# Kernel optimization log

Measured on AMD Instinct MI355X. Metric: run time of the kernel, lower is better.

Reference implementation:

```python
import jax, jax.numpy as jnp
import numpy as np

B, N, E = 8, 2000, 32000
LAT, STY, NF = 128, 64, 10
HEADS, HID = 4, 128
OUT = 3 + NF  # 13
EPS = 1e-5
SLOPE = 0.2


def _lin(k, fi, fo):
    return jax.random.normal(k, (fi, fo), dtype=jnp.float32) / np.sqrt(fi)


def setup_inputs() -> dict:
    key = jax.random.key(0)
    ks = jax.random.split(key, 32)
    inp = {
        'z': jax.random.normal(ks[0], (B, LAT), dtype=jnp.float32),
        'template_x': jax.random.normal(ks[1], (N, NF), dtype=jnp.float32),
        'template_edge_index': jax.random.randint(ks[2], (2, E), 0, N, dtype=jnp.int32),
        # style MLP
        'mlp_w1': _lin(ks[3], LAT, 256), 'mlp_b1': jnp.zeros((256,), jnp.float32),
        'mlp_w2': _lin(ks[4], 256, 512), 'mlp_b2': jnp.zeros((512,), jnp.float32),
        'mlp_w3': _lin(ks[5], 512, STY), 'mlp_b3': jnp.zeros((STY,), jnp.float32),
        # GAT1: in = NF + STY = 74 -> heads*HID = 512, concat
        'gat1_w': _lin(ks[6], NF + STY, HEADS * HID),
        'gat1_as': jax.random.normal(ks[7], (HEADS, HID), jnp.float32) * 0.1,
        'gat1_ad': jax.random.normal(ks[8], (HEADS, HID), jnp.float32) * 0.1,
        'gat1_b': jnp.zeros((HEADS * HID,), jnp.float32),
        'ln1_g': jnp.ones((HEADS * HID,), jnp.float32), 'ln1_b': jnp.zeros((HEADS * HID,), jnp.float32),
        # GAT2: 512 -> 512, concat
        'gat2_w': _lin(ks[9], HEADS * HID, HEADS * HID),
        'gat2_as': jax.random.normal(ks[10], (HEADS, HID), jnp.float32) * 0.1,
        'gat2_ad': jax.random.normal(ks[11], (HEADS, HID), jnp.float32) * 0.1,
        'gat2_b': jnp.zeros((HEADS * HID,), jnp.float32),
        'ln2_g': jnp.ones((HEADS * HID,), jnp.float32), 'ln2_b': jnp.zeros((HEADS * HID,), jnp.float32),
        # GAT3: 512 -> 13, 1 head, no concat
        'gat3_w': _lin(ks[12], HEADS * HID, OUT),
        'gat3_as': jax.random.normal(ks[13], (1, OUT), jnp.float32) * 0.1,
        'gat3_ad': jax.random.normal(ks[14], (1, OUT), jnp.float32) * 0.1,
        'gat3_b': jnp.zeros((OUT,), jnp.float32),
    }
    return inp


def gat_conv(x, src, dst, n_nodes, W, a_src, a_dst, bias, heads, out_ch, concat):
    # x: [NT, F_in]; per-head linear transform
    h = (x @ W).reshape(-1, heads, out_ch)              # [NT, H, C]
    als = jnp.sum(h * a_src[None], axis=-1)             # [NT, H]
    ald = jnp.sum(h * a_dst[None], axis=-1)             # [NT, H]
    logits = jax.nn.leaky_relu(als[src] + ald[dst], SLOPE)   # [E, H]
    # segment softmax over destination nodes (self-loops guarantee nonempty segments)
    mx = jax.ops.segment_max(logits, dst, num_segments=n_nodes)
    alpha = jnp.exp(logits - mx[dst])
    den = jax.ops.segment_sum(alpha, dst, num_segments=n_nodes)
    alpha = alpha / den[dst]                             # [E, H]
    msgs = h[src] * alpha[:, :, None]                    # [E, H, C]
    out = jax.ops.segment_sum(msgs, dst, num_segments=n_nodes)  # [NT, H, C]
    if concat:
        return out.reshape(n_nodes, heads * out_ch) + bias
    return out.mean(axis=1) + bias


def layer_norm(x, g, b):
    mu = jnp.mean(x, axis=-1, keepdims=True)
    var = jnp.mean((x - mu) ** 2, axis=-1, keepdims=True)
    return (x - mu) * jax.lax.rsqrt(var + EPS) * g + b


def reference(z, template_x, template_edge_index,
              mlp_w1, mlp_b1, mlp_w2, mlp_b2, mlp_w3, mlp_b3,
              gat1_w, gat1_as, gat1_ad, gat1_b, ln1_g, ln1_b,
              gat2_w, gat2_as, gat2_ad, gat2_b, ln2_g, ln2_b,
              gat3_w, gat3_as, gat3_ad, gat3_b):
    bsz = z.shape[0]
    n = template_x.shape[0]
    nt = bsz * n
    # batch the template graph: replicate nodes, offset edge indices per graph
    x = jnp.tile(template_x, (bsz, 1))                                  # [NT, NF]
    off = (jnp.arange(bsz, dtype=template_edge_index.dtype) * n)
    ei = (template_edge_index[:, None, :] + off[None, :, None]).reshape(2, -1)  # [2, B*E]
    loops = jnp.arange(nt, dtype=ei.dtype)
    src = jnp.concatenate([ei[0], loops])
    dst = jnp.concatenate([ei[1], loops])
    # style MLP
    s = jax.nn.leaky_relu(z @ mlp_w1 + mlp_b1, SLOPE)
    s = jax.nn.leaky_relu(s @ mlp_w2 + mlp_b2, SLOPE)
    s = s @ mlp_w3 + mlp_b3                                             # [B, STY]
    s_exp = jnp.repeat(s, n, axis=0)                                    # [NT, STY]
    H0 = jnp.concatenate([x, s_exp], axis=1)
    H1 = jax.nn.leaky_relu(gat_conv(H0, src, dst, nt, gat1_w, gat1_as, gat1_ad, gat1_b, HEADS, HID, True), SLOPE)
    H1n = layer_norm(H1, ln1_g, ln1_b)
    H2 = jax.nn.leaky_relu(gat_conv(H1n, src, dst, nt, gat2_w, gat2_as, gat2_ad, gat2_b, HEADS, HID, True), SLOPE)
    H2 = H2 + H1n
    H2n = layer_norm(H2, ln2_g, ln2_b)
    H_out = gat_conv(H2n, src, dst, nt, gat3_w, gat3_as, gat3_ad, gat3_b, 1, OUT, False)  # [NT, 13]
    delta_p = H_out[:, :3]
    delta_f = H_out[:, 3:]
    p_gen = x[:, :3] + delta_p
    X_gen = jnp.concatenate([p_gen, x[:, 3:] + delta_f[:, 3:]], axis=1)  # X[:, :3] overwritten by p_gen
    EF = p_gen[ei[1]] - p_gen[ei[0]]                                     # edge displacement vectors [B*E, 3]
    return X_gen, p_gen, EF
```

## Files before the change

### kernel.cpp

```cpp
#include <hip/hip_runtime.h>
#include <hip/hip_fp16.h>

constexpr int Bz = 8, Nn = 2000, Ee = 32000, NTOT = 16000;
constexpr int XG_OFF = 0, PG_OFF = 160000, EF_OFF = 208000;
#define SLOPE 0.2f
#define EPSL 1e-5f

typedef __attribute__((ext_vector_type(8))) _Float16 f16x8;
typedef __attribute__((ext_vector_type(4))) float float4v;

__device__ __forceinline__ float lrelu(float x) { return x > 0.f ? x : SLOPE * x; }

__device__ __forceinline__ unsigned short f2h(float x) {
  _Float16 hh = (_Float16)x;
  return *(unsigned short*)&hh;
}

__device__ __forceinline__ float wave_max(float v) {
  for (int o = 32; o; o >>= 1) v = fmaxf(v, __shfl_xor(v, o));
  return v;
}
__device__ __forceinline__ float wave_sum(float v) {
  for (int o = 32; o; o >>= 1) v += __shfl_xor(v, o);
  return v;
}

__global__ void hist_k(const int* __restrict__ tei, int* __restrict__ counts) {
  int j = blockIdx.x * 256 + threadIdx.x;
  if (j < Ee) atomicAdd(&counts[tei[Ee + j]], 1);
}

__global__ void scan_k(const int* __restrict__ counts, int* __restrict__ offs) {
  __shared__ int part[256];
  int t = threadIdx.x;
  int loc[8];
  int s = 0;
  for (int i = 0; i < 8; i++) {
    int idx = t * 8 + i;
    int c = (idx < Nn) ? counts[idx] : 0;
    loc[i] = s; s += c;
  }
  part[t] = s;
  __syncthreads();
  for (int o = 1; o < 256; o <<= 1) {
    int v = (t >= o) ? part[t - o] : 0;
    __syncthreads();
    part[t] += v;
    __syncthreads();
  }
  int excl = (t == 0) ? 0 : part[t - 1];
  for (int i = 0; i < 8; i++) {
    int idx = t * 8 + i;
    if (idx < Nn) offs[idx] = excl + loc[i];
  }
  if (t == 255) offs[Nn] = part[255];
}

__global__ void place_k(const int* __restrict__ tei, const int* __restrict__ offs,
                        int* __restrict__ cursor, int* __restrict__ colb) {
  int j = blockIdx.x * 256 + threadIdx.x;
  if (j < Ee) {
    int d = tei[Ee + j];
    int slot = offs[d] + atomicAdd(&cursor[d], 1);
    colb[slot] = tei[j];
  }
}

template <int K, int ACT>
__global__ __launch_bounds__(256) void lin_k(const float* __restrict__ x, const float* __restrict__ w,
                                             const float* __restrict__ bias, float* __restrict__ y,
                                             int O) {
  int gw = blockIdx.x * 4 + (threadIdx.x >> 6);
  int lane = threadIdx.x & 63;
  int bb = gw / O, o = gw - bb * O;
  float acc = 0.f;
#pragma unroll
  for (int k = lane; k < K; k += 64) acc += x[bb * K + k] * w[k * O + o];
  acc = wave_sum(acc);
  if (lane == 0) {
    if (bias) acc += bias[o];
    y[gw] = ACT ? lrelu(acc) : acc;
  }
}

__global__ __launch_bounds__(256) void w2bf_k(const float* __restrict__ W, unsigned short* __restrict__ Bt) {
  __shared__ float tile[32][33];
  int tx = threadIdx.x & 31, ty = threadIdx.x >> 5;
  int x0 = blockIdx.x * 32;
  int y0 = blockIdx.y * 32;
  for (int r = ty; r < 32; r += 8) tile[r][tx] = W[(y0 + r) * 512 + x0 + tx];
  __syncthreads();
  for (int r = ty; r < 32; r += 8) Bt[(x0 + r) * 512 + (y0 + tx)] = f2h(tile[tx][r]);
}

__global__ void w3t_k(const float* __restrict__ W, unsigned short* __restrict__ W3t) {
  for (int idx = threadIdx.x; idx < 8192; idx += 256) {
    int col = idx >> 9, k = idx & 511;
    float v = (col < 13) ? W[k * 13 + col] : 0.f;
    W3t[idx] = f2h(v);
  }
}

__global__ __launch_bounds__(256) void h1_k(const float* __restrict__ tx, const float* __restrict__ g1w,
                                            const float* __restrict__ pb,
                                            const float* __restrict__ a_s, const float* __restrict__ a_d,
                                            unsigned short* __restrict__ h1, float* __restrict__ als,
                                            float* __restrict__ ald) {
  int blk = blockIdx.x;
  int b = blk & 7, nl = blk >> 3;
  int n = b * Nn + nl;
  int head = threadIdx.x >> 6, lane = threadIdx.x & 63;
  int c = head * 128 + 2 * lane;
  float t0 = 0.f, t1 = 0.f;
#pragma unroll
  for (int k = 0; k < 10; k++) {
    float xv = tx[nl * 10 + k];
    float2 wv = *(const float2*)&g1w[k * 512 + c];
    t0 += xv * wv.x; t1 += xv * wv.y;
  }
  float2 pv = *(const float2*)&pb[b * 512 + c];
  float hx = t0 + pv.x, hy = t1 + pv.y;
  ushort2 st; st.x = f2h(hx); st.y = f2h(hy);
  *(ushort2*)&h1[(size_t)n * 512 + c] = st;
  float2 av = *(const float2*)&a_s[c];
  float2 dv = *(const float2*)&a_d[c];
  float pa = wave_sum(hx * av.x + hy * av.y);
  float pd = wave_sum(hx * dv.x + hy * dv.y);
  if (lane == 0) { als[n * 4 + head] = pa; ald[n * 4 + head] = pd; }
}

template <int RESID>
__global__ __launch_bounds__(256) void agg_k(const unsigned short* __restrict__ h,
                                             const float* __restrict__ als, const float* __restrict__ ald,
                                             const float* __restrict__ bias,
                                             const float* __restrict__ g, const float* __restrict__ beta,
                                             const unsigned short* __restrict__ resid,
                                             unsigned short* __restrict__ out,
                                             const int* __restrict__ offs, const int* __restrict__ colb) {
  int blk = blockIdx.x;
  int b = blk & 7, nl = blk >> 3;
  int n = b * Nn + nl;
  int w = threadIdx.x >> 6, lane = threadIdx.x & 63;
  int rs = offs[nl];
  int nit = offs[nl + 1] - rs + 1;
  float aldn = ald[n * 4 + w];

  __shared__ unsigned int alpha_u[4][68];
  __shared__ int sgn[64];
  __shared__ float part[4][512];
  __shared__ float invs[4];
  __shared__ float red[8];
  __shared__ float bcs[2];

  __half2 acc2[4];
#pragma unroll
  for (int j = 0; j < 4; j++) acc2[j] = __float2half2_rn(0.f);

  const unsigned short* hbase = h + lane * 8;
  int hd = lane >> 4;

  if (nit <= 64) {
    int sg = n;
    float logit = -3e38f;
    if (lane < nit) {
      sg = (lane < nit - 1) ? colb[rs + lane] + b * Nn : n;
      logit = lrelu(als[sg * 4 + w] + aldn);
      if (w == 0) sgn[lane] = sg;
    }
    float m = wave_max(logit);
    float raw = (lane < nit) ? __expf(logit - m) : 0.f;
    float den = wave_sum(raw);
    if (lane == 0) invs[w] = 1.f / den;
    __half2 a2 = __float2half2_rn(raw);
    alpha_u[w][lane] = *(unsigned int*)&a2;
    __syncthreads();
    int e = w;
    for (; e + 4 < nit; e += 8) {
      unsigned int au0 = alpha_u[hd][e];
      int sg0 = sgn[e];
      unsigned int au1 = alpha_u[hd][e + 4];
      int sg1 = sgn[e + 4];
      uint4 hv0 = *(const uint4*)(hbase + (size_t)sg0 * 512);
      uint4 hv1 = *(const uint4*)(hbase + (size_t)sg1 * 512);
      __half2 a0 = *(__half2*)&au0;
      __half2 a1 = *(__half2*)&au1;
      acc2[0] = __hfma2(a0, *(__half2*)&hv0.x, acc2[0]);
      acc2[1] = __hfma2(a0, *(__half2*)&hv0.y, acc2[1]);
      acc2[2] = __hfma2(a0, *(__half2*)&hv0.z, acc2[2]);
      acc2[3] = __hfma2(a0, *(__half2*)&hv0.w, acc2[3]);
      acc2[0] = __hfma2(a1, *(__half2*)&hv1.x, acc2[0]);
      acc2[1] = __hfma2(a1, *(__half2*)&hv1.y, acc2[1]);
      acc2[2] = __hfma2(a1, *(__half2*)&hv1.z, acc2[2]);
      acc2[3] = __hfma2(a1, *(__half2*)&hv1.w, acc2[3]);
    }
    if (e < nit) {
      unsigned int au0 = alpha_u[hd][e];
      int sg0 = sgn[e];
      uint4 hv0 = *(const uint4*)(hbase + (size_t)sg0 * 512);
      __half2 a0 = *(__half2*)&au0;
      acc2[0] = __hfma2(a0, *(__half2*)&hv0.x, acc2[0]);
      acc2[1] = __hfma2(a0, *(__half2*)&hv0.y, acc2[1]);
      acc2[2] = __hfma2(a0, *(__half2*)&hv0.z, acc2[2]);
      acc2[3] = __hfma2(a0, *(__half2*)&hv0.w, acc2[3]);
    }
  } else {
    float m = -3e38f;
    for (int i = lane; i < nit; i += 64) {
      int sg = (i < nit - 1) ? colb[rs + i] + b * Nn : n;
      m = fmaxf(m, lrelu(als[sg * 4 + w] + aldn));
    }
    m = wave_max(m);
    float den = 0.f;
    for (int base = 0; base < nit; base += 64) {
      int cnt = min(64, nit - base);
      int sg = n;
      float raw = 0.f;
      if (lane < cnt) {
        int i = base + lane;
        sg = (i < nit - 1) ? colb[rs + i] + b * Nn : n;
        raw = __expf(lrelu(als[sg * 4 + w] + aldn) - m);
        if (w == 0) sgn[lane] = sg;
      }
      den += raw;
      __half2 a2 = __float2half2_rn(raw);
      alpha_u[w][lane] = *(unsigned int*)&a2;
      __syncthreads();
      for (int e = w; e < cnt; e += 4) {
        unsigned int au = alpha_u[hd][e];
        int sge = sgn[e];
        uint4 hv = *(const uint4*)(hbase + (size_t)sge * 512);
        __half2 a2e = *(__half2*)&au;
        acc2[0] = __hfma2(a2e, *(__half2*)&hv.x, acc2[0]);
        acc2[1] = __hfma2(a2e, *(__half2*)&hv.y, acc2[1]);
        acc2[2] = __hfma2(a2e, *(__half2*)&hv.z, acc2[2]);
        acc2[3] = __hfma2(a2e, *(__half2*)&hv.w, acc2[3]);
      }
      __syncthreads();
    }
    den = wave_sum(den);
    if (lane == 0) invs[w] = 1.f / den;
  }

  float fv[8];
#pragma unroll
  for (int j = 0; j < 4; j++) {
    float2 f2 = __half22float2(acc2[j]);
    fv[2 * j] = f2.x; fv[2 * j + 1] = f2.y;
  }
  *(float4*)&part[w][lane * 8] = make_float4(fv[0], fv[1], fv[2], fv[3]);
  *(float4*)&part[w][lane * 8 + 4] = make_float4(fv[4], fv[5], fv[6], fv[7]);
  __syncthreads();

  int c = 2 * (int)threadIdx.x;
  float inv = invs[c >> 7];
  float s0 = part[0][c] + part[1][c] + part[2][c] + part[3][c];
  float s1 = part[0][c + 1] + part[1][c + 1] + part[2][c + 1] + part[3][c + 1];
  float v0 = lrelu(s0 * inv + bias[c]);
  float v1 = lrelu(s1 * inv + bias[c + 1]);
  if (RESID) {
    unsigned int rv = *(const unsigned int*)&resid[(size_t)n * 512 + c];
    __half2 rh = *(__half2*)&rv;
    float2 rf = __half22float2(rh);
    v0 += rf.x; v1 += rf.y;
  }
  float p1 = wave_sum(v0 + v1);
  float p2 = wave_sum(v0 * v0 + v1 * v1);
  if (lane == 0) { red[w] = p1; red[4 + w] = p2; }
  __syncthreads();
  if (threadIdx.x == 0) {
    float s1r = red[0] + red[1] + red[2] + red[3];
    float s2r = red[4] + red[5] + red[6] + red[7];
    float mu = s1r * (1.f / 512.f);
    float var = s2r * (1.f / 512.f) - mu * mu;
    bcs[0] = mu;
    bcs[1] = rsqrtf(var + EPSL);
  }
  __syncthreads();
  float mu = bcs[0], rstd = bcs[1];
  float o0 = (v0 - mu) * rstd * g[c] + beta[c];
  float o1 = (v1 - mu) * rstd * g[c + 1] + beta[c + 1];
  ushort2 st; st.x = f2h(o0); st.y = f2h(o1);
  *(ushort2*)&out[(size_t)n * 512 + c] = st;
}

__global__ __launch_bounds__(512) void gemm2_k(const unsigned short* __restrict__ A,
                                               const unsigned short* __restrict__ Bt,
                                               unsigned short* __restrict__ C,
                                               const float* __restrict__ As, const float* __restrict__ Ad,
                                               float* __restrict__ als2, float* __restrict__ ald2) {
  __shared__ char smem[73728];
  char* sAc = smem;
  char* sBc = smem + 8192;
  int t = threadIdx.x;
  int lane = t & 63, w = t >> 6;
  int wm = w >> 2, wn = w & 3;
  int m0 = blockIdx.x * 64;

  float4v acc[2][8];
#pragma unroll
  for (int i = 0; i < 2; i++)
#pragma unroll
    for (int j = 0; j < 8; j++) acc[i][j] = (float4v){0.f, 0.f, 0.f, 0.f};

  int arow = t >> 3, aklin = (t & 7) * 16;
  int asw = arow * 128 + (aklin ^ ((arow & 7) << 4));
  int brow[8], bklin[8], bsw[8];
#pragma unroll
  for (int i = 0; i < 8; i++) {
    int slot = i * 512 + t;
    brow[i] = slot >> 3;
    bklin[i] = (slot & 7) * 16;
    bsw[i] = brow[i] * 128 + (bklin[i] ^ ((brow[i] & 7) << 4));
  }

  uint4 va = *(const uint4*)((const char*)A + (size_t)(m0 + arow) * 1024 + aklin);
  uint4 vb[8];
#pragma unroll
  for (int i = 0; i < 8; i++)
    vb[i] = *(const uint4*)((const char*)Bt + (size_t)brow[i] * 1024 + bklin[i]);

  int r_a = wm * 32 + (lane & 15);
  int r_b = wn * 128 + (lane & 15);
  int kbb = (lane >> 4) * 16;
  int sw = ((lane & 15) & 7) << 4;

  for (int k0 = 0; k0 < 512; k0 += 64) {
    if (k0) __syncthreads();
    *(uint4*)(sAc + asw) = va;
#pragma unroll
    for (int i = 0; i < 8; i++) *(uint4*)(sBc + bsw[i]) = vb[i];
    __syncthreads();
    if (k0 + 64 < 512) {
      va = *(const uint4*)((const char*)A + (size_t)(m0 + arow) * 1024 + (k0 + 64) * 2 + aklin);
#pragma unroll
      for (int i = 0; i < 8; i++)
        vb[i] = *(const uint4*)((const char*)Bt + (size_t)brow[i] * 1024 + (k0 + 64) * 2 + bklin[i]);
    }
#pragma unroll
    for (int ksub = 0; ksub < 2; ksub++) {
      f16x8 af[2], bg[8];
#pragma unroll
      for (int m = 0; m < 2; m++)
        af[m] = *(const f16x8*)(sAc + (r_a + m * 16) * 128 + ((ksub * 64 + kbb) ^ sw));
#pragma unroll
      for (int nn = 0; nn < 8; nn++)
        bg[nn] = *(const f16x8*)(sBc + (r_b + nn * 16) * 128 + ((ksub * 64 + kbb) ^ sw));
#pragma unroll
      for (int m = 0; m < 2; m++)
#pragma unroll
        for (int nn = 0; nn < 8; nn++)
          acc[m][nn] = __builtin_amdgcn_mfma_f32_16x16x32_f16(af[m], bg[nn], acc[m][nn], 0, 0, 0);
    }
  }

  {
    float asv[8], adv[8];
#pragma unroll
    for (int nn = 0; nn < 8; nn++) {
      asv[nn] = As[wn * 128 + nn * 16 + (lane & 15)];
      adv[nn] = Ad[wn * 128 + nn * 16 + (lane & 15)];
    }
#pragma unroll
    for (int m = 0; m < 2; m++) {
#pragma unroll
      for (int r = 0; r < 4; r++) {
        float pa = 0.f, pd = 0.f;
#pragma unroll
        for (int nn = 0; nn < 8; nn++) { pa += acc[m][nn][r] * asv[nn]; pd += acc[m][nn][r] * adv[nn]; }
        for (int o = 1; o < 16; o <<= 1) { pa += __shfl_xor(pa, o); pd += __shfl_xor(pd, o); }
        if ((lane & 15) == 0) {
          int row = m0 + wm * 32 + (lane >> 4) * 4 + m * 16 + r;
          als2[row * 4 + wn] = pa;
          ald2[row * 4 + wn] = pd;
        }
      }
    }
  }

  __syncthreads();
  unsigned short* sC = (unsigned short*)smem;
  int rbase = wm * 32 + (lane >> 4) * 4;
  int cbase = wn * 128 + (lane & 15);
#pragma unroll
  for (int m = 0; m < 2; m++)
#pragma unroll
    for (int nn = 0; nn < 8; nn++)
#pragma unroll
      for (int r = 0; r < 4; r++)
        sC[(rbase + m * 16 + r) * 520 + cbase + nn * 16] = f2h(acc[m][nn][r]);
  __syncthreads();
#pragma unroll
  for (int p = 0; p < 8; p++) {
    int row = p * 8 + (t >> 6);
    int co = (t & 63) * 8;
    uint4 v = *(const uint4*)&sC[row * 520 + co];
    *(uint4*)&C[(size_t)(m0 + row) * 512 + co] = v;
  }
}

__global__ __launch_bounds__(256) void gemm3_k(const unsigned short* __restrict__ H,
                                               const unsigned short* __restrict__ W3t,
                                               const float* __restrict__ as3, const float* __restrict__ ad3,
                                               float* __restrict__ h3, float* __restrict__ als3,
                                               float* __restrict__ ald3) {
  int w = threadIdx.x >> 6, l = threadIdx.x & 63;
  int m0 = blockIdx.x * 64 + w * 16;
  int r16 = l & 15, g4 = l >> 4;
  float4v acc = (float4v){0.f, 0.f, 0.f, 0.f};
  const unsigned short* ha = H + (size_t)(m0 + r16) * 512 + g4 * 8;
  const unsigned short* wb = W3t + (size_t)r16 * 512 + g4 * 8;
#pragma unroll
  for (int kk = 0; kk < 16; kk++) {
    f16x8 a = *(const f16x8*)(ha + kk * 32);
    f16x8 bfr = *(const f16x8*)(wb + kk * 32);
    acc = __builtin_amdgcn_mfma_f32_16x16x32_f16(a, bfr, acc, 0, 0, 0);
  }
  int col = r16;
  float asv = (col < 13) ? as3[col] : 0.f;
  float adv = (col < 13) ? ad3[col] : 0.f;
#pragma unroll
  for (int r = 0; r < 4; r++) {
    float v = acc[r];
    int row = m0 + g4 * 4 + r;
    if (col < 13) h3[row * 13 + col] = v;
    float sa = v * asv, sd = v * adv;
    for (int o = 1; o < 16; o <<= 1) { sa += __shfl_xor(sa, o); sd += __shfl_xor(sd, o); }
    if (col == 0) { als3[row] = sa; ald3[row] = sd; }
  }
}

__global__ __launch_bounds__(64) void agg3_k(const float* __restrict__ h3, const float* __restrict__ als3,
                                             const float* __restrict__ ald3, const float* __restrict__ b3,
                                             const float* __restrict__ tx, const int* __restrict__ offs,
                                             const int* __restrict__ colb, float* __restrict__ dout) {
  int blk = blockIdx.x, lane = threadIdx.x;
  int b = blk & 7, nl = blk >> 3;
  int n = b * Nn + nl;
  int rs = offs[nl], deg = offs[nl + 1] - rs;
  float aldn = ald3[n];
  float sl = lrelu(als3[n] + aldn);
  float a = 0.f, inv;
  if (deg <= 64) {
    int sgl = 0; float logit = -1e30f;
    if (lane < deg) { sgl = colb[rs + lane] + b * Nn; logit = lrelu(als3[sgl] + aldn); }
    float m = wave_max(fmaxf(logit, sl));
    float raw = (lane < deg) ? __expf(logit - m) : 0.f;
    float es = __expf(sl - m);
    inv = 1.f / (wave_sum(raw) + es);
    if (lane < 13) a = es * h3[n * 13 + lane];
    for (int e = 0; e < deg; e++) {
      float w = __shfl(raw, e);
      int sg = __shfl(sgl, e);
      if (lane < 13) a += w * h3[sg * 13 + lane];
    }
  } else {
    float m = sl;
    for (int e = lane; e < deg; e += 64) {
      int sg = colb[rs + e] + b * Nn;
      m = fmaxf(m, lrelu(als3[sg] + aldn));
    }
    m = wave_max(m);
    float es = __expf(sl - m);
    float den = (lane == 0) ? es : 0.f;
    if (lane < 13) a = es * h3[n * 13 + lane];
    for (int base = 0; base < deg; base += 64) {
      int cnt = min(64, deg - base);
      int sgl = 0; float raw = 0.f;
      if (lane < cnt) {
        sgl = colb[rs + base + lane] + b * Nn;
        raw = __expf(lrelu(als3[sgl] + aldn) - m);
      }
      den += raw;
      for (int e = 0; e < cnt; e++) {
        float w = __shfl(raw, e);
        int sg = __shfl(sgl, e);
        if (lane < 13) a += w * h3[sg * 13 + lane];
      }
    }
    inv = 1.f / wave_sum(den);
  }
  a *= inv;
  float hv = a + ((lane < 13) ? b3[lane] : 0.f);
  float txv = (lane < 10) ? tx[nl * 10 + lane] : 0.f;
  float pv = txv + hv;
  if (lane < 3) dout[PG_OFF + n * 3 + lane] = pv;
  float up = __shfl(hv, lane + 3);
  float xg = (lane < 3) ? pv : (txv + up);
  if (lane < 10) dout[XG_OFF + n * 10 + lane] = xg;
}

__global__ void ef_k(const int* __restrict__ tei, float* __restrict__ dout) {
  int e = blockIdx.x * 256 + threadIdx.x;
  int b = e / Ee, j = e - b * Ee;
  int sg = tei[j] + b * Nn;
  int dg = tei[Ee + j] + b * Nn;
  const float* pg = dout + PG_OFF;
  dout[EF_OFF + e * 3 + 0] = pg[dg * 3 + 0] - pg[sg * 3 + 0];
  dout[EF_OFF + e * 3 + 1] = pg[dg * 3 + 1] - pg[sg * 3 + 1];
  dout[EF_OFF + e * 3 + 2] = pg[dg * 3 + 2] - pg[sg * 3 + 2];
}

extern "C" void kernel_launch(void* const* d_in, const int* in_sizes, int n_in,
                              void* d_out, int out_size, void* d_ws, size_t ws_size,
                              hipStream_t stream) {
  const float* z = (const float*)d_in[0];
  const float* tx = (const float*)d_in[1];
  const int* tei = (const int*)d_in[2];
  const float* w1 = (const float*)d_in[3];
  const float* b1 = (const float*)d_in[4];
  const float* w2 = (const float*)d_in[5];
  const float* b2 = (const float*)d_in[6];
  const float* w3 = (const float*)d_in[7];
  const float* b3 = (const float*)d_in[8];
  const float* g1w = (const float*)d_in[9];
  const float* g1as = (const float*)d_in[10];
  const float* g1ad = (const float*)d_in[11];
  const float* g1b = (const float*)d_in[12];
  const float* ln1g = (const float*)d_in[13];
  const float* ln1b = (const float*)d_in[14];
  const float* g2w = (const float*)d_in[15];
  const float* g2as = (const float*)d_in[16];
  const float* g2ad = (const float*)d_in[17];
  const float* g2b = (const float*)d_in[18];
  const float* ln2g = (const float*)d_in[19];
  const float* ln2b = (const float*)d_in[20];
  const float* g3w = (const float*)d_in[21];
  const float* g3as = (const float*)d_in[22];
  const float* g3ad = (const float*)d_in[23];
  const float* g3b = (const float*)d_in[24];
  float* out = (float*)d_out;

  float* F = (float*)d_ws;
  float* pb_ = F + 0;
  float* l1_ = F + 8192;
  float* l2_ = F + 16384;
  float* s_ = F + 24576;
  float* als1 = F + 100000;
  float* ald1 = F + 164000;
  float* als2 = F + 228000;
  float* ald2 = F + 292000;
  float* als3 = F + 356000;
  float* ald3 = F + 372000;
  float* h3_ = F + 388000;
  unsigned short* U = (unsigned short*)(F + 600000);
  unsigned short* hA = U;
  unsigned short* hB = U + 8192000;
  unsigned short* Bt = U + 16384000;
  unsigned short* W3t = U + 16646144;
  int* I = (int*)(F + 10000000);
  int* counts = I;
  int* cursor = I + 2000;
  int* offs = I + 4000;
  int* colb = I + 6001;

  hipMemsetAsync(counts, 0, 4000 * sizeof(int), stream);
  hist_k<<<125, 256, 0, stream>>>(tei, counts);
  scan_k<<<1, 256, 0, stream>>>(counts, offs);
  place_k<<<125, 256, 0, stream>>>(tei, offs, cursor, colb);

  w2bf_k<<<dim3(16, 16), 256, 0, stream>>>(g2w, Bt);
  w3t_k<<<1, 256, 0, stream>>>(g3w, W3t);

  lin_k<128, 1><<<512, 256, 0, stream>>>(z, w1, b1, l1_, 256);
  lin_k<256, 1><<<1024, 256, 0, stream>>>(l1_, w2, b2, l2_, 512);
  lin_k<512, 0><<<128, 256, 0, stream>>>(l2_, w3, b3, s_, 64);
  lin_k<64, 0><<<1024, 256, 0, stream>>>(s_, g1w + 10 * 512, nullptr, pb_, 512);

  h1_k<<<NTOT, 256, 0, stream>>>(tx, g1w, pb_, g1as, g1ad, hA, als1, ald1);
  agg_k<0><<<NTOT, 256, 0, stream>>>(hA, als1, ald1, g1b, ln1g, ln1b, nullptr, hB, offs, colb);

  gemm2_k<<<250, 512, 0, stream>>>(hB, Bt, hA, g2as, g2ad, als2, ald2);
  agg_k<1><<<NTOT, 256, 0, stream>>>(hA, als2, ald2, g2b, ln2g, ln2b, hB, hB, offs, colb);

  gemm3_k<<<250, 256, 0, stream>>>(hB, W3t, g3as, g3ad, h3_, als3, ald3);
  agg3_k<<<NTOT, 64, 0, stream>>>(h3_, als3, ald3, g3b, tx, offs, colb, out);
  ef_k<<<1000, 256, 0, stream>>>(tei, out);
}
```

Baseline: 216.5 us.

## Interleave GEMM and edge-kernel blocks by batch for cross-XCD cache locality

```diff
diff --git a/kernel.cpp b/kernel.cpp
--- a/kernel.cpp
+++ b/kernel.cpp
@@ -294,30 +294,34 @@
   int t = threadIdx.x;
   int lane = t & 63, w = t >> 6;
   int wm = w >> 2, wn = w & 3;
-  int m0 = blockIdx.x * 64;
+  int blk = blockIdx.x;
+  int b = blk & 7, i = blk >> 3;
+  int rows = min(64, Nn - i * 64);
+  int m0 = b * Nn + i * 64;
 
   float4v acc[2][8];
 #pragma unroll
-  for (int i = 0; i < 2; i++)
-#pragma unroll
-    for (int j = 0; j < 8; j++) acc[i][j] = (float4v){0.f, 0.f, 0.f, 0.f};
+  for (int q = 0; q < 2; q++)
+#pragma unroll
+    for (int j = 0; j < 8; j++) acc[q][j] = (float4v){0.f, 0.f, 0.f, 0.f};
 
   int arow = t >> 3, aklin = (t & 7) * 16;
   int asw = arow * 128 + (aklin ^ ((arow & 7) << 4));
+  int arow_c = m0 + min(arow, rows - 1);
   int brow[8], bklin[8], bsw[8];
 #pragma unroll
-  for (int i = 0; i < 8; i++) {
-    int slot = i * 512 + t;
-    brow[i] = slot >> 3;
-    bklin[i] = (slot & 7) * 16;
-    bsw[i] = brow[i] * 128 + (bklin[i] ^ ((brow[i] & 7) << 4));
-  }
-
-  uint4 va = *(const uint4*)((const char*)A + (size_t)(m0 + arow) * 1024 + aklin);
+  for (int q = 0; q < 8; q++) {
+    int slot = q * 512 + t;
+    brow[q] = slot >> 3;
+    bklin[q] = (slot & 7) * 16;
+    bsw[q] = brow[q] * 128 + (bklin[q] ^ ((brow[q] & 7) << 4));
+  }
+
+  uint4 va = *(const uint4*)((const char*)A + (size_t)arow_c * 1024 + aklin);
   uint4 vb[8];
 #pragma unroll
-  for (int i = 0; i < 8; i++)
-    vb[i] = *(const uint4*)((const char*)Bt + (size_t)brow[i] * 1024 + bklin[i]);
+  for (int q = 0; q < 8; q++)
+    vb[q] = *(const uint4*)((const char*)Bt + (size_t)brow[q] * 1024 + bklin[q]);
 
   int r_a = wm * 32 + (lane & 15);
   int r_b = wn * 128 + (lane & 15);
@@ -328,13 +332,13 @@
     if (k0) __syncthreads();
     *(uint4*)(sAc + asw) = va;
 #pragma unroll
-    for (int i = 0; i < 8; i++) *(uint4*)(sBc + bsw[i]) = vb[i];
+    for (int q = 0; q < 8; q++) *(uint4*)(sBc + bsw[q]) = vb[q];
     __syncthreads();
     if (k0 + 64 < 512) {
-      va = *(const uint4*)((const char*)A + (size_t)(m0 + arow) * 1024 + (k0 + 64) * 2 + aklin);
-#pragma unroll
-      for (int i = 0; i < 8; i++)
-        vb[i] = *(const uint4*)((const char*)Bt + (size_t)brow[i] * 1024 + (k0 + 64) * 2 + bklin[i]);
+      va = *(const uint4*)((const char*)A + (size_t)arow_c * 1024 + (k0 + 64) * 2 + aklin);
+#pragma unroll
+      for (int q = 0; q < 8; q++)
+        vb[q] = *(const uint4*)((const char*)Bt + (size_t)brow[q] * 1024 + (k0 + 64) * 2 + bklin[q]);
     }
 #pragma unroll
     for (int ksub = 0; ksub < 2; ksub++) {
@@ -368,10 +372,10 @@
 #pragma unroll
         for (int nn = 0; nn < 8; nn++) { pa += acc[m][nn][r] * asv[nn]; pd += acc[m][nn][r] * adv[nn]; }
         for (int o = 1; o < 16; o <<= 1) { pa += __shfl_xor(pa, o); pd += __shfl_xor(pd, o); }
-        if ((lane & 15) == 0) {
-          int row = m0 + wm * 32 + (lane >> 4) * 4 + m * 16 + r;
-          als2[row * 4 + wn] = pa;
-          ald2[row * 4 + wn] = pd;
+        int lrow = wm * 32 + (lane >> 4) * 4 + m * 16 + r;
+        if ((lane & 15) == 0 && lrow < rows) {
+          als2[(m0 + lrow) * 4 + wn] = pa;
+          ald2[(m0 + lrow) * 4 + wn] = pd;
         }
       }
     }
@@ -392,9 +396,11 @@
 #pragma unroll
   for (int p = 0; p < 8; p++) {
     int row = p * 8 + (t >> 6);
-    int co = (t & 63) * 8;
-    uint4 v = *(const uint4*)&sC[row * 520 + co];
-    *(uint4*)&C[(size_t)(m0 + row) * 512 + co] = v;
+    if (row < rows) {
+      int co = (t & 63) * 8;
+      uint4 v = *(const uint4*)&sC[row * 520 + co];
+      *(uint4*)&C[(size_t)(m0 + row) * 512 + co] = v;
+    }
   }
 }
 
@@ -404,10 +410,13 @@
                                                float* __restrict__ h3, float* __restrict__ als3,
                                                float* __restrict__ ald3) {
   int w = threadIdx.x >> 6, l = threadIdx.x & 63;
-  int m0 = blockIdx.x * 64 + w * 16;
+  int blk = blockIdx.x;
+  int b = blk & 7, i = blk >> 3;
+  int base = i * 64 + w * 16;
   int r16 = l & 15, g4 = l >> 4;
+  int lrow_ld = min(base + r16, Nn - 1);
   float4v acc = (float4v){0.f, 0.f, 0.f, 0.f};
-  const unsigned short* ha = H + (size_t)(m0 + r16) * 512 + g4 * 8;
+  const unsigned short* ha = H + (size_t)(b * Nn + lrow_ld) * 512 + g4 * 8;
   const unsigned short* wb = W3t + (size_t)r16 * 512 + g4 * 8;
 #pragma unroll
   for (int kk = 0; kk < 16; kk++) {
@@ -421,11 +430,14 @@
 #pragma unroll
   for (int r = 0; r < 4; r++) {
     float v = acc[r];
-    int row = m0 + g4 * 4 + r;
-    if (col < 13) h3[row * 13 + col] = v;
-    float sa = v * asv, sd = v * adv;
-    for (int o = 1; o < 16; o <<= 1) { sa += __shfl_xor(sa, o); sd += __shfl_xor(sd, o); }
-    if (col == 0) { als3[row] = sa; ald3[row] = sd; }
+    int lrow = base + g4 * 4 + r;
+    if (lrow < Nn) {
+      int row = b * Nn + lrow;
+      if (col < 13) h3[row * 13 + col] = v;
+      float sa = v * asv, sd = v * adv;
+      for (int o = 1; o < 16; o <<= 1) { sa += __shfl_xor(sa, o); sd += __shfl_xor(sd, o); }
+      if (col == 0) { als3[row] = sa; ald3[row] = sd; }
+    }
   }
 }
 
@@ -490,8 +502,10 @@
 }
 
 __global__ void ef_k(const int* __restrict__ tei, float* __restrict__ dout) {
-  int e = blockIdx.x * 256 + threadIdx.x;
-  int b = e / Ee, j = e - b * Ee;
+  int blk = blockIdx.x;
+  int b = blk & 7, i = blk >> 3;
+  int j = i * 256 + threadIdx.x;
+  int e = b * Ee + j;
   int sg = tei[j] + b * Nn;
   int dg = tei[Ee + j] + b * Nn;
   const float* pg = dout + PG_OFF;
@@ -569,10 +583,10 @@
   h1_k<<<NTOT, 256, 0, stream>>>(tx, g1w, pb_, g1as, g1ad, hA, als1, ald1);
   agg_k<0><<<NTOT, 256, 0, stream>>>(hA, als1, ald1, g1b, ln1g, ln1b, nullptr, hB, offs, colb);
 
-  gemm2_k<<<250, 512, 0, stream>>>(hB, Bt, hA, g2as, g2ad, als2, ald2);
+  gemm2_k<<<256, 512, 0, stream>>>(hB, Bt, hA, g2as, g2ad, als2, ald2);
   agg_k<1><<<NTOT, 256, 0, stream>>>(hA, als2, ald2, g2b, ln2g, ln2b, hB, hB, offs, colb);
 
-  gemm3_k<<<250, 256, 0, stream>>>(hB, W3t, g3as, g3ad, h3_, als3, ald3);
+  gemm3_k<<<256, 256, 0, stream>>>(hB, W3t, g3as, g3ad, h3_, als3, ald3);
   agg3_k<<<NTOT, 64, 0, stream>>>(h3_, als3, ald3, g3b, tx, offs, colb, out);
   ef_k<<<1000, 256, 0, stream>>>(tei, out);
 }
```

Result: no change. 216.2 us (-0.1%).
